# Optimization experiments

Measured on AMD Instinct MI355X. Metric: run time of the kernel, lower is better.

## Reference

```python
import jax, jax.numpy as jnp
import numpy as np

CTX_LEN = 2048
DK = 128
SEQ = 8192


def setup_inputs() -> dict:
    key = jax.random.key(0)
    kx, kq, kk, kv = jax.random.split(key, 4)
    x = jax.random.normal(kx, (SEQ, CTX_LEN), dtype=jnp.float32)
    # module initializes weights as rand(ctxLen, dk) * 0.05
    wq = jax.random.uniform(kq, (CTX_LEN, DK), dtype=jnp.float32) * 0.05
    wk = jax.random.uniform(kk, (CTX_LEN, DK), dtype=jnp.float32) * 0.05
    wv = jax.random.uniform(kv, (CTX_LEN, DK), dtype=jnp.float32) * 0.05
    return {"x": x, "wq": wq, "wk": wk, "wv": wv}


def reference(x, wq, wk, wv):
    dk = wq.shape[1]
    q = x @ wq          # [S, dk]
    k = x @ wk          # [S, dk]
    v = x @ wv          # [S, dk]
    # NOTE: source multiplies by sqrt(dk) (not the usual divide)
    scores = jnp.einsum("sd,td->st", q, k) * jnp.sqrt(jnp.float32(dk))  # [S, S]
    # NOTE: source softmax over dim=0 (column-wise)
    attn = jax.nn.softmax(scores, axis=0)
    return attn @ v     # [S, dk]
```

## Files before the change

kernel.cpp:

```cpp
#include <hip/hip_runtime.h>
#include <stdint.h>

#define SEQ 8192
#define CTX 2048
#define DK  128

typedef __attribute__((ext_vector_type(8))) __bf16 bf16x8;
typedef __attribute__((ext_vector_type(4))) float f32x4;
typedef unsigned short u16;

__device__ __forceinline__ u16 f2bf(float f) {
  unsigned int u = __builtin_bit_cast(unsigned int, f);
  u += 0x7FFFu + ((u >> 16) & 1u);
  return (u16)(u >> 16);
}
__device__ __forceinline__ u16 f2bf_fast(float f) {
  unsigned int u = __builtin_bit_cast(unsigned int, f);
  return (u16)((u + 0x8000u) >> 16);
}
__device__ __forceinline__ float bf2f(u16 h) {
  unsigned int u = ((unsigned int)h) << 16;
  return __builtin_bit_cast(float, u);
}
__device__ __forceinline__ void gl_lds16(const void* g, void* l) {
  __builtin_amdgcn_global_load_lds((__attribute__((address_space(1))) void*)g,
                                   (__attribute__((address_space(3))) void*)l, 16, 0, 0);
}
__device__ __forceinline__ f32x4 mfma16(bf16x8 a, bf16x8 b, f32x4 c) {
  return __builtin_amdgcn_mfma_f32_16x16x32_bf16(a, b, c, 0, 0, 0);
}

__global__ __launch_bounds__(256) void k_cvt_x(const float* __restrict__ x, u16* __restrict__ xb) {
  int i = blockIdx.x * 256 + threadIdx.x;
  float4 a = ((const float4*)x)[i];
  ushort4 r;
  r.x = f2bf(a.x); r.y = f2bf(a.y); r.z = f2bf(a.z); r.w = f2bf(a.w);
  ((ushort4*)xb)[i] = r;
}

__global__ __launch_bounds__(256) void k_cvt_w(const float* __restrict__ wq, const float* __restrict__ wk,
                                               const float* __restrict__ wv, u16* __restrict__ wT) {
  int mat = blockIdx.y;
  const float* w = mat == 0 ? wq : (mat == 1 ? wk : wv);
  float scale = (mat == 0) ? 11.313708498984761f : 1.0f;
  int tk = blockIdx.x & 63, tn = blockIdx.x >> 6;
  __shared__ float t[32][33];
  int tx = threadIdx.x & 31, ty = threadIdx.x >> 5;
  int k0 = tk * 32, n0 = tn * 32;
#pragma unroll
  for (int j = 0; j < 4; j++) {
    int kk = ty + j * 8;
    t[kk][tx] = w[(size_t)(k0 + kk) * DK + n0 + tx] * scale;
  }
  __syncthreads();
  u16* o = wT + (size_t)mat * DK * CTX;
#pragma unroll
  for (int j = 0; j < 4; j++) {
    int nn = ty + j * 8;
    o[(size_t)(n0 + nn) * CTX + k0 + tx] = f2bf(t[tx][nn]);
  }
}

__global__ __launch_bounds__(256, 2) void k_qkv(const u16* __restrict__ xb, const u16* __restrict__ wT,
                                                u16* __restrict__ qb, u16* __restrict__ kb, u16* __restrict__ vb) {
  __shared__ __align__(16) u16 As[2][8192];
  __shared__ __align__(16) u16 Bs[2][8192];
  int bid = blockIdx.x;
  int xcd = bid & 7, j = bid >> 3;
  int mat = j % 3, mb = xcd * 8 + j / 3;
  const u16* B = wT + (size_t)mat * DK * CTX;
  u16* C = mat == 0 ? qb : (mat == 1 ? kb : vb);
  int tid = threadIdx.x, lane = tid & 63, w = tid >> 6;
  int r15 = lane & 15, gq = lane >> 4;
  int wr = w >> 1, wc = w & 1;
  int gqx = gq ^ ((r15 >> 1) & 3);

  auto stage = [&](int buf, int k0) {
#pragma unroll
    for (int i = 0; i < 4; i++) {
      int c = i * 256 + tid;
      int kd = c >> 9, row = (c >> 2) & 127, cc = (c & 3) ^ ((c >> 3) & 3);
      gl_lds16(xb + (size_t)(mb * 128 + row) * CTX + k0 + kd * 32 + cc * 8, &As[buf][(i * 256 + w * 64) * 8]);
    }
#pragma unroll
    for (int i = 0; i < 4; i++) {
      int c = i * 256 + tid;
      int kd = c >> 9, row = (c >> 2) & 127, cc = (c & 3) ^ ((c >> 3) & 3);
      gl_lds16(B + (size_t)row * CTX + k0 + kd * 32 + cc * 8, &Bs[buf][(i * 256 + w * 64) * 8]);
    }
  };

  f32x4 acc[4][4] = {};
  stage(0, 0);
  asm volatile("s_waitcnt vmcnt(0)" ::: "memory");
  __syncthreads();
  for (int it = 0; it < 32; ++it) {
    int buf = it & 1;
    if (it < 31) stage(buf ^ 1, it * 64 + 64);
    bf16x8 af[2][4], bfr[2][4];
#pragma unroll
    for (int kd = 0; kd < 2; kd++)
#pragma unroll
      for (int mi = 0; mi < 4; mi++)
        af[kd][mi] = *(const bf16x8*)&As[buf][kd * 4096 + (wr * 64 + mi * 16 + r15) * 32 + gqx * 8];
#pragma unroll
    for (int kd = 0; kd < 2; kd++)
#pragma unroll
      for (int ni = 0; ni < 4; ni++)
        bfr[kd][ni] = *(const bf16x8*)&Bs[buf][kd * 4096 + (wc * 64 + ni * 16 + r15) * 32 + gqx * 8];
#pragma unroll
    for (int mi = 0; mi < 4; mi++)
#pragma unroll
      for (int ni = 0; ni < 4; ni++) {
        acc[mi][ni] = mfma16(af[0][mi], bfr[0][ni], acc[mi][ni]);
        acc[mi][ni] = mfma16(af[1][mi], bfr[1][ni], acc[mi][ni]);
      }
    asm volatile("s_waitcnt vmcnt(0)" ::: "memory");
    __syncthreads();
  }
#pragma unroll
  for (int mi = 0; mi < 4; mi++)
#pragma unroll
    for (int ni = 0; ni < 4; ni++)
#pragma unroll
      for (int rr = 0; rr < 4; rr++) {
        int mrow = mb * 128 + wr * 64 + mi * 16 + gq * 4 + rr;
        int ncol = wc * 64 + ni * 16 + r15;
        C[(size_t)mrow * DK + ncol] = f2bf(acc[mi][ni][rr]);
      }
}

__global__ __launch_bounds__(256, 2) void k_p2(const u16* __restrict__ qb, const u16* __restrict__ kb,
                                               float* __restrict__ m_part, float* __restrict__ z_part) {
  __shared__ __align__(16) u16 Ks2[16384];
  __shared__ __align__(16) u16 Qs2[2][8192];
  const float L2E = 1.4426950408889634f;
  int bid = blockIdx.x;
  int ss = bid & 7, tb = bid >> 3;
  int t0 = tb * 128, s0 = ss * 1024;
  int tid = threadIdx.x, lane = tid & 63, w = tid >> 6;
  int r15 = lane & 15, gq = lane >> 4;
  int gqx = gq ^ ((r15 >> 1) & 3);

  auto stageQ = [&](int buf, int sc) {
#pragma unroll
    for (int i = 0; i < 4; i++) {
      int c = i * 256 + tid;
      int kd = c >> 8, row = (c >> 2) & 63, cc = (c & 3) ^ ((c >> 3) & 3);
      gl_lds16(qb + (size_t)(s0 + sc + row) * DK + kd * 32 + cc * 8, &Qs2[buf][(i * 256 + w * 64) * 8]);
    }
  };

#pragma unroll
  for (int i = 0; i < 8; i++) {
    int c = i * 256 + tid;
    int kd = c >> 9, row = (c >> 2) & 127, cc = (c & 3) ^ ((c >> 3) & 3);
    gl_lds16(kb + (size_t)(t0 + row) * DK + kd * 32 + cc * 8, &Ks2[(i * 256 + w * 64) * 8]);
  }
  stageQ(0, 0);
  asm volatile("s_waitcnt vmcnt(0)" ::: "memory");
  __syncthreads();
  bf16x8 af[2][4];
#pragma unroll
  for (int mi = 0; mi < 2; mi++)
#pragma unroll
    for (int kd = 0; kd < 4; kd++)
      af[mi][kd] = *(const bf16x8*)&Ks2[kd * 4096 + (w * 32 + mi * 16 + r15) * 32 + gqx * 8];
  float runM[8], runZ[8];
#pragma unroll
  for (int jj = 0; jj < 8; jj++) { runM[jj] = -3.0e38f; runZ[jj] = 0.f; }

  for (int sc = 0; sc < 1024; sc += 64) {
    int buf = (sc >> 6) & 1;
    if (sc < 960) stageQ(buf ^ 1, sc + 64);
    f32x4 pacc[4][2] = {};
#pragma unroll
    for (int ni = 0; ni < 4; ni++)
#pragma unroll
      for (int kd = 0; kd < 4; kd++) {
        bf16x8 bq = *(const bf16x8*)&Qs2[buf][kd * 2048 + (ni * 16 + r15) * 32 + gqx * 8];
        pacc[ni][0] = mfma16(af[0][kd], bq, pacc[ni][0]);
        pacc[ni][1] = mfma16(af[1][kd], bq, pacc[ni][1]);
      }
#pragma unroll
    for (int mi = 0; mi < 2; mi++)
#pragma unroll
      for (int rr = 0; rr < 4; rr++) {
        int jj = mi * 4 + rr;
        float m8 = fmaxf(fmaxf(pacc[0][mi][rr], pacc[1][mi][rr]),
                         fmaxf(pacc[2][mi][rr], pacc[3][mi][rr])) * L2E;
        if (m8 > runM[jj] - 60.f) {
          float nm = fmaxf(runM[jj], m8);
          float z = runZ[jj] * __builtin_amdgcn_exp2f(runM[jj] - nm);
#pragma unroll
          for (int ni = 0; ni < 4; ni++)
            z += __builtin_amdgcn_exp2f(fmaf(pacc[ni][mi][rr], L2E, -nm));
          runZ[jj] = z; runM[jj] = nm;
        }
      }
    asm volatile("s_waitcnt vmcnt(0)" ::: "memory");
    __syncthreads();
  }
#pragma unroll
  for (int d = 1; d < 16; d <<= 1) {
#pragma unroll
    for (int jj = 0; jj < 8; jj++) {
      float oM = __shfl_xor(runM[jj], d);
      float oZ = __shfl_xor(runZ[jj], d);
      float nm = fmaxf(runM[jj], oM);
      runZ[jj] = runZ[jj] * __builtin_amdgcn_exp2f(runM[jj] - nm) + oZ * __builtin_amdgcn_exp2f(oM - nm);
      runM[jj] = nm;
    }
  }
  if (r15 == 0) {
#pragma unroll
    for (int mi = 0; mi < 2; mi++)
#pragma unroll
      for (int rr = 0; rr < 4; rr++) {
        int t = t0 + w * 32 + mi * 16 + gq * 4 + rr;
        m_part[ss * SEQ + t] = runM[mi * 4 + rr];
        z_part[ss * SEQ + t] = runZ[mi * 4 + rr];
      }
  }
}

__global__ __launch_bounds__(256) void k_p2c(const float* __restrict__ m_part, const float* __restrict__ z_part,
                                             const u16* __restrict__ vb, float* __restrict__ mL,
                                             u16* __restrict__ vT) {
  int t0 = blockIdx.x * 64;
  int tid = threadIdx.x;
  __shared__ float rz[64];
  __shared__ __align__(16) u16 vt[64 * DK];
  if (tid < 64) {
    int t = t0 + tid;
    float m0 = -3.0e38f, z = 0.f;
#pragma unroll
    for (int p = 0; p < 8; p++) {
      float a = m_part[p * SEQ + t], b = z_part[p * SEQ + t];
      float nm = fmaxf(m0, a);
      z = z * __builtin_amdgcn_exp2f(m0 - nm) + b * __builtin_amdgcn_exp2f(a - nm);
      m0 = nm;
    }
    mL[t] = m0;
    rz[tid] = 1.0f / z;
  }
  const uint4* vs = (const uint4*)(vb + (size_t)t0 * DK);
  uint4* vd = (uint4*)vt;
#pragma unroll
  for (int i = 0; i < 4; i++) vd[i * 256 + tid] = vs[i * 256 + tid];
  __syncthreads();
  int d = tid >> 1, half = tid & 1;
#pragma unroll
  for (int jj = 0; jj < 32; jj++) {
    int tl = half * 32 + jj;
    float f = bf2f(vt[tl * DK + d]) * rz[tl];
    vT[(size_t)d * SEQ + t0 + tl] = f2bf(f);
  }
}

__global__ __launch_bounds__(256, 2) void k_p3(const u16* __restrict__ qb, const u16* __restrict__ kb,
                                               const u16* __restrict__ vT, const float* __restrict__ mLg,
                                               float* __restrict__ outp) {
  __shared__ __align__(16) u16 Ks2[8192];
  __shared__ __align__(16) u16 Vs2[2][8192];
  __shared__ __align__(16) u16 Ps[2 * 128 * 40];
  const float L2E = 1.4426950408889634f;
  int bid = blockIdx.x;
  int ts = bid & 7, sb = bid >> 3;
  int s0 = sb * 128, tbase = ts * 1024;
  int tid = threadIdx.x, lane = tid & 63, w = tid >> 6;
  int r15 = lane & 15, gq = lane >> 4;
  int wr = w >> 1, wc = w & 1;
  int gqx = gq ^ ((r15 >> 1) & 3);

  auto stageK = [&](int tc) {
#pragma unroll
    for (int i = 0; i < 4; i++) {
      int c = i * 256 + tid;
      int kd = c >> 8, t = (c >> 2) & 63, cc = (c & 3) ^ ((c >> 3) & 3);
      gl_lds16(kb + (size_t)(tbase + tc + t) * DK + kd * 32 + cc * 8, &Ks2[(i * 256 + w * 64) * 8]);
    }
  };
  auto stageV = [&](int buf, int tc) {
#pragma unroll
    for (int i = 0; i < 4; i++) {
      int c = i * 256 + tid;
      int kt = c >> 9, d = (c >> 2) & 127, cc = (c & 3) ^ ((c >> 3) & 3);
      gl_lds16(vT + (size_t)d * SEQ + tbase + tc + kt * 32 + cc * 8, &Vs2[buf][(i * 256 + w * 64) * 8]);
    }
  };

  bf16x8 qf[2][4];
#pragma unroll
  for (int ni = 0; ni < 2; ni++)
#pragma unroll
    for (int kd = 0; kd < 4; kd++)
      qf[ni][kd] = *(const bf16x8*)(qb + (size_t)(s0 + w * 32 + ni * 16 + r15) * DK + kd * 32 + gq * 8);

  stageK(0);
  stageV(0, 0);
  asm volatile("s_waitcnt vmcnt(0)" ::: "memory");
  __syncthreads();

  f32x4 o[4][4] = {};
  for (int tc = 0; tc < 1024; tc += 64) {
    int vbuf = (tc >> 6) & 1;
    float4 mv4[4];
#pragma unroll
    for (int mi = 0; mi < 4; mi++)
      mv4[mi] = *(const float4*)(mLg + tbase + tc + mi * 16 + gq * 4);
#pragma unroll
    for (int mi = 0; mi < 4; mi++) {
      bf16x8 a4[4];
#pragma unroll
      for (int kd = 0; kd < 4; kd++)
        a4[kd] = *(const bf16x8*)&Ks2[kd * 2048 + (mi * 16 + r15) * 32 + gqx * 8];
      f32x4 p0 = {}, p1 = {};
#pragma unroll
      for (int kd = 0; kd < 4; kd++) {
        p0 = mfma16(a4[kd], qf[0][kd], p0);
        p1 = mfma16(a4[kd], qf[1][kd], p1);
      }
      ushort4 pk0, pk1;
      {
        float e;
        float mv0 = mv4[mi].x, mv1 = mv4[mi].y, mv2 = mv4[mi].z, mv3 = mv4[mi].w;
        e = __builtin_amdgcn_exp2f(fmaf(p0[0], L2E, -mv0)); pk0.x = f2bf_fast(e);
        e = __builtin_amdgcn_exp2f(fmaf(p0[1], L2E, -mv1)); pk0.y = f2bf_fast(e);
        e = __builtin_amdgcn_exp2f(fmaf(p0[2], L2E, -mv2)); pk0.z = f2bf_fast(e);
        e = __builtin_amdgcn_exp2f(fmaf(p0[3], L2E, -mv3)); pk0.w = f2bf_fast(e);
        e = __builtin_amdgcn_exp2f(fmaf(p1[0], L2E, -mv0)); pk1.x = f2bf_fast(e);
        e = __builtin_amdgcn_exp2f(fmaf(p1[1], L2E, -mv1)); pk1.y = f2bf_fast(e);
        e = __builtin_amdgcn_exp2f(fmaf(p1[2], L2E, -mv2)); pk1.z = f2bf_fast(e);
        e = __builtin_amdgcn_exp2f(fmaf(p1[3], L2E, -mv3)); pk1.w = f2bf_fast(e);
      }
      int ktp = mi >> 1;
      int w32 = (mi & 1) * 16 + gq * 4;
      *(ushort4*)&Ps[ktp * 5120 + (w * 32 + r15) * 40 + w32] = pk0;
      *(ushort4*)&Ps[ktp * 5120 + (w * 32 + 16 + r15) * 40 + w32] = pk1;
    }
    __syncthreads();
    if (tc < 960) {
      stageK(tc + 64);
      stageV(vbuf ^ 1, tc + 64);
    }
#pragma unroll
    for (int kt = 0; kt < 2; kt++) {
      bf16x8 pa[4], vv[4];
#pragma unroll
      for (int mi2 = 0; mi2 < 4; mi2++)
        pa[mi2] = *(const bf16x8*)&Ps[kt * 5120 + (wr * 64 + mi2 * 16 + r15) * 40 + gq * 8];
#pragma unroll
      for (int ni2 = 0; ni2 < 4; ni2++)
        vv[ni2] = *(const bf16x8*)&Vs2[vbuf][kt * 4096 + (wc * 64 + ni2 * 16 + r15) * 32 + gqx * 8];
#pragma unroll
      for (int mi2 = 0; mi2 < 4; mi2++)
#pragma unroll
        for (int ni2 = 0; ni2 < 4; ni2++)
          o[mi2][ni2] = mfma16(pa[mi2], vv[ni2], o[mi2][ni2]);
    }
    asm volatile("s_waitcnt vmcnt(0)" ::: "memory");
    __syncthreads();
  }
  float* dst = outp + (size_t)ts * SEQ * DK;
#pragma unroll
  for (int mi2 = 0; mi2 < 4; mi2++)
#pragma unroll
    for (int ni2 = 0; ni2 < 4; ni2++)
#pragma unroll
      for (int rr = 0; rr < 4; rr++) {
        int srow = s0 + wr * 64 + mi2 * 16 + gq * 4 + rr;
        int dcol = wc * 64 + ni2 * 16 + r15;
        dst[(size_t)srow * DK + dcol] = o[mi2][ni2][rr];
      }
}

__global__ __launch_bounds__(256) void k_p4(const float* __restrict__ outp, float* __restrict__ out) {
  int i = blockIdx.x * 256 + threadIdx.x;
  const float4* s = (const float4*)outp;
  float4 a = s[i];
#pragma unroll
  for (int p = 1; p < 8; p++) {
    float4 b = s[(size_t)p * 262144 + i];
    a.x += b.x; a.y += b.y; a.z += b.z; a.w += b.w;
  }
  ((float4*)out)[i] = a;
}

extern "C" void kernel_launch(void* const* d_in, const int* in_sizes, int n_in,
                              void* d_out, int out_size, void* d_ws, size_t ws_size,
                              hipStream_t stream) {
  (void)in_sizes; (void)n_in; (void)out_size; (void)ws_size;
  const float* x  = (const float*)d_in[0];
  const float* wq = (const float*)d_in[1];
  const float* wk = (const float*)d_in[2];
  const float* wv = (const float*)d_in[3];
  float* out = (float*)d_out;

  char* wsb = (char*)d_ws;
  u16*   xb    = (u16*)wsb;
  float* outp  = (float*)wsb;
  u16*   wT    = (u16*)(wsb + 33554432);
  u16*   qb    = (u16*)(wsb + 35127296);
  u16*   kb    = (u16*)(wsb + 37224448);
  u16*   vb    = (u16*)(wsb + 39321600);
  u16*   vT    = (u16*)(wsb + 41418752);
  float* mLf   = (float*)(wsb + 43515904);
  float* mpart = (float*)(wsb + 43548672);
  float* zpart = (float*)(wsb + 43810816);

  k_cvt_x<<<16384, 256, 0, stream>>>(x, xb);
  k_cvt_w<<<dim3(256, 3), 256, 0, stream>>>(wq, wk, wv, wT);
  k_qkv<<<192, 256, 0, stream>>>(xb, wT, qb, kb, vb);
  k_p2<<<512, 256, 0, stream>>>(qb, kb, mpart, zpart);
  k_p2c<<<128, 256, 0, stream>>>(mpart, zpart, vb, mLf, vT);
  k_p3<<<512, 256, 0, stream>>>(qb, kb, vT, mLf, outp);
  k_p4<<<1024, 256, 0, stream>>>(outp, out);
}
```

Baseline: 217.1 us.

## Fuse x fp32-to-bf16 conversion into QKV GEMM and raise wave priority in P·V

```diff
diff --git a/kernel.cpp b/kernel.cpp
--- a/kernel.cpp
+++ b/kernel.cpp
@@ -28,14 +28,6 @@
 }
 __device__ __forceinline__ f32x4 mfma16(bf16x8 a, bf16x8 b, f32x4 c) {
   return __builtin_amdgcn_mfma_f32_16x16x32_bf16(a, b, c, 0, 0, 0);
-}
-
-__global__ __launch_bounds__(256) void k_cvt_x(const float* __restrict__ x, u16* __restrict__ xb) {
-  int i = blockIdx.x * 256 + threadIdx.x;
-  float4 a = ((const float4*)x)[i];
-  ushort4 r;
-  r.x = f2bf(a.x); r.y = f2bf(a.y); r.z = f2bf(a.z); r.w = f2bf(a.w);
-  ((ushort4*)xb)[i] = r;
 }
 
 __global__ __launch_bounds__(256) void k_cvt_w(const float* __restrict__ wq, const float* __restrict__ wk,
@@ -61,27 +53,22 @@
   }
 }
 
-__global__ __launch_bounds__(256, 2) void k_qkv(const u16* __restrict__ xb, const u16* __restrict__ wT,
+__global__ __launch_bounds__(256, 3) void k_qkv(const float* __restrict__ x, const u16* __restrict__ wT,
                                                 u16* __restrict__ qb, u16* __restrict__ kb, u16* __restrict__ vb) {
-  __shared__ __align__(16) u16 As[2][8192];
+  __shared__ __align__(16) u16 As[2][4096];
   __shared__ __align__(16) u16 Bs[2][8192];
   int bid = blockIdx.x;
-  int xcd = bid & 7, j = bid >> 3;
-  int mat = j % 3, mb = xcd * 8 + j / 3;
+  int sid = (bid & 7) * 48 + (bid >> 3);
+  int mat = sid >> 7, mb = sid & 127;
   const u16* B = wT + (size_t)mat * DK * CTX;
   u16* C = mat == 0 ? qb : (mat == 1 ? kb : vb);
   int tid = threadIdx.x, lane = tid & 63, w = tid >> 6;
   int r15 = lane & 15, gq = lane >> 4;
-  int wr = w >> 1, wc = w & 1;
+  int wr = w & 1, wc = w >> 1;
   int gqx = gq ^ ((r15 >> 1) & 3);
-
-  auto stage = [&](int buf, int k0) {
-#pragma unroll
-    for (int i = 0; i < 4; i++) {
-      int c = i * 256 + tid;
-      int kd = c >> 9, row = (c >> 2) & 127, cc = (c & 3) ^ ((c >> 3) & 3);
-      gl_lds16(xb + (size_t)(mb * 128 + row) * CTX + k0 + kd * 32 + cc * 8, &As[buf][(i * 256 + w * 64) * 8]);
-    }
+  int arow = tid >> 2, af4 = tid & 3;
+
+  auto stageB = [&](int buf, int k0) {
 #pragma unroll
     for (int i = 0; i < 4; i++) {
       int c = i * 256 + tid;
@@ -89,42 +76,67 @@
       gl_lds16(B + (size_t)row * CTX + k0 + kd * 32 + cc * 8, &Bs[buf][(i * 256 + w * 64) * 8]);
     }
   };
-
-  f32x4 acc[4][4] = {};
-  stage(0, 0);
+  auto loadA = [&](int k0, float4* ar) {
+#pragma unroll
+    for (int rr = 0; rr < 4; rr++) {
+      int f4 = af4 + rr * 4;
+      ar[rr] = *(const float4*)(x + (size_t)(mb * 64 + arow) * CTX + k0 + f4 * 4);
+    }
+  };
+  auto writeA = [&](int buf, const float4* ar) {
+#pragma unroll
+    for (int rr = 0; rr < 4; rr++) {
+      int f4 = af4 + rr * 4;
+      int kd = f4 >> 3, g8 = (f4 >> 1) & 3, inner = (f4 & 1) * 4;
+      int g8x = g8 ^ ((arow >> 1) & 3);
+      ushort4 v;
+      v.x = f2bf(ar[rr].x); v.y = f2bf(ar[rr].y); v.z = f2bf(ar[rr].z); v.w = f2bf(ar[rr].w);
+      *(ushort4*)&As[buf][kd * 2048 + arow * 32 + g8x * 8 + inner] = v;
+    }
+  };
+
+  f32x4 acc[2][4] = {};
+  float4 ar[4];
+  stageB(0, 0);
+  loadA(0, ar);
+  writeA(0, ar);
   asm volatile("s_waitcnt vmcnt(0)" ::: "memory");
   __syncthreads();
   for (int it = 0; it < 32; ++it) {
     int buf = it & 1;
-    if (it < 31) stage(buf ^ 1, it * 64 + 64);
-    bf16x8 af[2][4], bfr[2][4];
+    if (it < 31) {
+      stageB(buf ^ 1, it * 64 + 64);
+      loadA(it * 64 + 64, ar);
+    }
+    bf16x8 af[2][2], bfr[2][4];
 #pragma unroll
     for (int kd = 0; kd < 2; kd++)
 #pragma unroll
-      for (int mi = 0; mi < 4; mi++)
-        af[kd][mi] = *(const bf16x8*)&As[buf][kd * 4096 + (wr * 64 + mi * 16 + r15) * 32 + gqx * 8];
+      for (int mi = 0; mi < 2; mi++)
+        af[kd][mi] = *(const bf16x8*)&As[buf][kd * 2048 + (wr * 32 + mi * 16 + r15) * 32 + gqx * 8];
 #pragma unroll
     for (int kd = 0; kd < 2; kd++)
 #pragma unroll
       for (int ni = 0; ni < 4; ni++)
         bfr[kd][ni] = *(const bf16x8*)&Bs[buf][kd * 4096 + (wc * 64 + ni * 16 + r15) * 32 + gqx * 8];
 #pragma unroll
-    for (int mi = 0; mi < 4; mi++)
+    for (int mi = 0; mi < 2; mi++)
 #pragma unroll
       for (int ni = 0; ni < 4; ni++) {
         acc[mi][ni] = mfma16(af[0][mi], bfr[0][ni], acc[mi][ni]);
         acc[mi][ni] = mfma16(af[1][mi], bfr[1][ni], acc[mi][ni]);
       }
+    if (it < 31) writeA(buf ^ 1, ar);
     asm volatile("s_waitcnt vmcnt(0)" ::: "memory");
     __syncthreads();
   }
 #pragma unroll
-  for (int mi = 0; mi < 4; mi++)
+  for (int mi = 0; mi < 2; mi++)
 #pragma unroll
     for (int ni = 0; ni < 4; ni++)
 #pragma unroll
       for (int rr = 0; rr < 4; rr++) {
-        int mrow = mb * 128 + wr * 64 + mi * 16 + gq * 4 + rr;
+        int mrow = mb * 64 + wr * 32 + mi * 16 + gq * 4 + rr;
         int ncol = wc * 64 + ni * 16 + r15;
         C[(size_t)mrow * DK + ncol] = f2bf(acc[mi][ni][rr]);
       }
@@ -344,6 +356,7 @@
       stageK(tc + 64);
       stageV(vbuf ^ 1, tc + 64);
     }
+    __builtin_amdgcn_s_setprio(1);
 #pragma unroll
     for (int kt = 0; kt < 2; kt++) {
       bf16x8 pa[4], vv[4];
@@ -359,6 +372,7 @@
         for (int ni2 = 0; ni2 < 4; ni2++)
           o[mi2][ni2] = mfma16(pa[mi2], vv[ni2], o[mi2][ni2]);
     }
+    __builtin_amdgcn_s_setprio(0);
     asm volatile("s_waitcnt vmcnt(0)" ::: "memory");
     __syncthreads();
   }
@@ -398,7 +412,6 @@
   float* out = (float*)d_out;
 
   char* wsb = (char*)d_ws;
-  u16*   xb    = (u16*)wsb;
   float* outp  = (float*)wsb;
   u16*   wT    = (u16*)(wsb + 33554432);
   u16*   qb    = (u16*)(wsb + 35127296);
@@ -409,9 +422,8 @@
   float* mpart = (float*)(wsb + 43548672);
   float* zpart = (float*)(wsb + 43810816);
 
-  k_cvt_x<<<16384, 256, 0, stream>>>(x, xb);
   k_cvt_w<<<dim3(256, 3), 256, 0, stream>>>(wq, wk, wv, wT);
-  k_qkv<<<192, 256, 0, stream>>>(xb, wT, qb, kb, vb);
+  k_qkv<<<384, 256, 0, stream>>>(x, wT, qb, kb, vb);
   k_p2<<<512, 256, 0, stream>>>(qb, kb, mpart, zpart);
   k_p2c<<<128, 256, 0, stream>>>(mpart, zpart, vb, mLf, vT);
   k_p3<<<512, 256, 0, stream>>>(qb, kb, vT, mLf, outp);
```

After: 214.6 us. Within noise of the previous version (-1.2%).
